# Kernel optimization log

Measured on AMD Instinct MI355X. Metric: run time of the kernel, lower is better.

## Reference

```python
import jax, jax.numpy as jnp
import numpy as np

EPS = 1e-12

def setup_inputs() -> dict:
    key = jax.random.key(0)
    k1, k2 = jax.random.split(key)
    B, C, H, W = 16, 256, 64, 64
    x1 = jax.random.normal(k1, (B, C, H, W), dtype=jnp.float32)
    x2 = jax.random.normal(k2, (B, C, H, W), dtype=jnp.float32)
    return {"x1": x1, "x2": x2}

def _l2norm(x):
    # F.normalize(p=2, dim=2, eps=1e-12): divide by max(norm, eps)
    n = jnp.linalg.norm(x, axis=2, keepdims=True)
    return x / jnp.maximum(n, EPS)

def reference(x1, x2):
    B, C, H, W = x1.shape
    x111 = x1.reshape(B, C, H * W)            # [B,C,N]
    x211 = x2.reshape(B, C, H * W)
    x11 = _l2norm(x111)
    x21 = _l2norm(x211)
    # four CxC score matmuls, fused pairwise adds
    attn1 = jnp.einsum('bcn,bdn->bcd', x11, x11)
    attn2 = jnp.einsum('bcn,bdn->bcd', x21, x21)
    attn0 = jnp.einsum('bcn,bdn->bcd', x21, x11)
    attn00 = jnp.einsum('bcn,bdn->bcd', x11, x21)
    attn11 = jax.nn.softmax(attn1 + attn0, axis=-1)   # [B,C,C]
    attn22 = jax.nn.softmax(attn2 + attn00, axis=-1)
    # back-projection, torch transpose(1,2).reshape(B,C,H,W) semantics
    y1 = jnp.einsum('bcd,bdn->bcn', attn11, x111)     # [B,C,N]
    y2 = jnp.einsum('bcd,bdn->bcn', attn22, x211)
    x1_o = jnp.swapaxes(y1, 1, 2).reshape(B, C, H, W) + x1
    x2_o = jnp.swapaxes(y2, 1, 2).reshape(B, C, H, W) + x2
    return x1_o + x2_o
```

## Files before the change

### kernel.cpp

```cpp
#include <hip/hip_runtime.h>
#include <hip/hip_bf16.h>

#define B_ 16
#define C_ 256
#define N_ 4096
#define CN_ (C_ * N_)

typedef __attribute__((ext_vector_type(8))) short bf16x8_t;
typedef __attribute__((ext_vector_type(8))) unsigned short u16x8_t;
typedef __attribute__((ext_vector_type(4))) float f32x4_t;
typedef unsigned int u32;
typedef unsigned short u16;

__device__ __forceinline__ u16 f2bf(float f) {
    __hip_bfloat16 h = __float2bfloat16(f);
    return __builtin_bit_cast(u16, h);
}
__device__ __forceinline__ float bf2f(u16 u) {
    return __builtin_bit_cast(float, (u32)u << 16);
}

__device__ __forceinline__ void gl_lds16(const void* g, void* l) {
    __builtin_amdgcn_global_load_lds(
        (const __attribute__((address_space(1))) u32*)(g),
        (__attribute__((address_space(3))) u32*)(l), 16, 0, 0);
}

__global__ __launch_bounds__(256) void knorm(const float* __restrict__ x1,
                                             const float* __restrict__ x2,
                                             u16* __restrict__ x1n,
                                             u16* __restrict__ x2n,
                                             u16* __restrict__ sN,
                                             u16* __restrict__ sxb,
                                             float* __restrict__ norms) {
    __shared__ float sx1[4096];
    __shared__ float sx2[4096];
    int row = blockIdx.x;
    int t = threadIdx.x;
    const float4* r1 = (const float4*)(x1 + (size_t)row * N_);
    const float4* r2 = (const float4*)(x2 + (size_t)row * N_);
    float s1 = 0.f, s2 = 0.f;
#pragma unroll
    for (int p = 0; p < 4; ++p) {
        float4 a = r1[p * 256 + t];
        float4 b = r2[p * 256 + t];
        s1 += a.x * a.x + a.y * a.y + a.z * a.z + a.w * a.w;
        s2 += b.x * b.x + b.y * b.y + b.z * b.z + b.w * b.w;
        *(float4*)&sx1[(p * 256 + t) * 4] = a;
        *(float4*)&sx2[(p * 256 + t) * 4] = b;
    }
#pragma unroll
    for (int m = 32; m; m >>= 1) { s1 += __shfl_xor(s1, m); s2 += __shfl_xor(s2, m); }
    __shared__ float red[2][4];
    int wid = t >> 6;
    if ((t & 63) == 0) { red[0][wid] = s1; red[1][wid] = s2; }
    __syncthreads();
    s1 = red[0][0] + red[0][1] + red[0][2] + red[0][3];
    s2 = red[1][0] + red[1][1] + red[1][2] + red[1][3];
    float n1 = fmaxf(sqrtf(s1), 1e-12f);
    float n2 = fmaxf(sqrtf(s2), 1e-12f);
    if (t == 0) {
        int bb = row >> 8, cc = row & 255;
        norms[(bb * 2 + 0) * 256 + cc] = n1;
        norms[(bb * 2 + 1) * 256 + cc] = n2;
    }
    float i1 = 1.0f / n1, i2 = 1.0f / n2;
    const size_t rbase = (size_t)row * N_;
#pragma unroll
    for (int j = 0; j < 2; ++j) {
        int e = j * 2048 + t * 8;
        float a[8], b[8];
        *(float4*)&a[0] = *(const float4*)&sx1[e];
        *(float4*)&a[4] = *(const float4*)&sx1[e + 4];
        *(float4*)&b[0] = *(const float4*)&sx2[e];
        *(float4*)&b[4] = *(const float4*)&sx2[e + 4];
        u16x8_t w1, w2, ws, wr;
#pragma unroll
        for (int i = 0; i < 8; ++i) {
            float va = a[i] * i1, vb = b[i] * i2;
            w1[i] = f2bf(va);
            w2[i] = f2bf(vb);
            ws[i] = f2bf(va + vb);
            wr[i] = f2bf(a[i] + b[i]);
        }
        *(u16x8_t*)(x1n + rbase + e) = w1;
        *(u16x8_t*)(x2n + rbase + e) = w2;
        *(u16x8_t*)(sN  + rbase + e) = ws;
        *(u16x8_t*)(sxb + rbase + e) = wr;
    }
}

__global__ __launch_bounds__(256) void klogits(const u16* __restrict__ sN,
                                               const u16* __restrict__ x1n,
                                               const u16* __restrict__ x2n,
                                               float* __restrict__ part) {
    int bid = blockIdx.x;
    int xcd = bid & 7;
    int u = bid >> 3;
    int b = xcd + 8 * (u & 1);
    int tile = (u >> 1) & 15;
    int kc4 = u >> 5;
    int c0 = (tile & 3) * 64;
    int d0 = (tile >> 2) * 64;

    __shared__ u16 lds[2][3 * 4096];

    int t = threadIdx.x, lane = t & 63, wid = t >> 6;
    int w = wid & 1, chalf = wid >> 1;

    const char* tb[3];
    tb[0] = (const char*)(sN  + (size_t)b * CN_ + (size_t)c0 * N_ + kc4 * 1024);
    tb[1] = (const char*)(x1n + (size_t)b * CN_ + (size_t)d0 * N_ + kc4 * 1024);
    tb[2] = (const char*)(x2n + (size_t)b * CN_ + (size_t)d0 * N_ + kc4 * 1024);
    const char* gsrc[6];
    int ldoff[6];
#pragma unroll
    for (int qq = 0; qq < 6; ++qq) {
        int q = wid * 6 + qq;
        int ti = q >> 3;
        int s0 = (q & 7) * 1024 + lane * 16;
        int rrow = s0 >> 7, inner = s0 & 127;
        gsrc[qq] = tb[ti] + (size_t)rrow * (N_ * 2) + (inner ^ ((rrow & 7) << 4));
        ldoff[qq] = q * 1024;
    }

    f32x4_t acc[2][4];
#pragma unroll
    for (int i = 0; i < 2; ++i)
#pragma unroll
        for (int j = 0; j < 4; ++j) acc[i][j] = 0.f;

    int kl = (lane >> 4) * 16;
    int rA0 = chalf * 32 + (lane & 15);

#pragma unroll
    for (int qq = 0; qq < 6; ++qq)
        gl_lds16(gsrc[qq], (char*)lds[0] + ldoff[qq]);
    __syncthreads();

    for (int ks = 0; ks < 16; ++ks) {
        int p = ks & 1;
        if (ks < 15) {
            int kbyte = (ks + 1) * 128;
#pragma unroll
            for (int qq = 0; qq < 6; ++qq)
                gl_lds16(gsrc[qq] + kbyte, (char*)lds[p ^ 1] + ldoff[qq]);
        }
        const char* Abase = (const char*)lds[p];
        const char* Bbase = (const char*)lds[p] + (1 + w) * 8192;
#pragma unroll
        for (int ksub = 0; ksub < 2; ++ksub) {
            int kc = ksub * 64 + kl;
            bf16x8_t af[2], bfr[4];
#pragma unroll
            for (int mi = 0; mi < 2; ++mi) {
                int rr = rA0 + mi * 16;
                af[mi] = *(const bf16x8_t*)(Abase + ((rr << 7) + (kc ^ ((rr & 7) << 4))));
            }
#pragma unroll
            for (int ni = 0; ni < 4; ++ni) {
                int rr = ni * 16 + (lane & 15);
                bfr[ni] = *(const bf16x8_t*)(Bbase + ((rr << 7) + (kc ^ ((rr & 7) << 4))));
            }
#pragma unroll
            for (int mi = 0; mi < 2; ++mi)
#pragma unroll
                for (int ni = 0; ni < 4; ++ni)
                    acc[mi][ni] = __builtin_amdgcn_mfma_f32_16x16x32_bf16(af[mi], bfr[ni], acc[mi][ni], 0, 0, 0);
        }
        __syncthreads();
    }

    float* outp = part + ((((size_t)kc4 * 16 + b) * 2 + w) * 256 + c0 + chalf * 32) * 256 + d0;
    int orow = (lane >> 4) * 4, ocol = lane & 15;
#pragma unroll
    for (int mi = 0; mi < 2; ++mi)
#pragma unroll
        for (int ni = 0; ni < 4; ++ni)
#pragma unroll
            for (int r = 0; r < 4; ++r)
                outp[(size_t)(mi * 16 + orow + r) * 256 + ni * 16 + ocol] = acc[mi][ni][r];
}

__global__ __launch_bounds__(256) void ksoftmax(const float* __restrict__ part,
                                                const float* __restrict__ norms,
                                                u16* __restrict__ attnp) {
    const size_t S = 2097152;
    int rid = blockIdx.x * 4 + (threadIdx.x >> 6);
    int l = threadIdx.x & 63;
    int bw = rid >> 8, c = rid & 255;
    size_t rbase = (size_t)bw * 65536 + (size_t)c * 256;
    float v[4];
    float m = -1e30f;
#pragma unroll
    for (int j = 0; j < 4; ++j) {
        int d = j * 64 + l;
        v[j] = part[rbase + d] + part[rbase + S + d] +
               part[rbase + 2 * S + d] + part[rbase + 3 * S + d];
        m = fmaxf(m, v[j]);
    }
#pragma unroll
    for (int s = 32; s; s >>= 1) m = fmaxf(m, __shfl_xor(m, s));
    float sum = 0.f;
#pragma unroll
    for (int j = 0; j < 4; ++j) { v[j] = __expf(v[j] - m); sum += v[j]; }
#pragma unroll
    for (int s = 32; s; s >>= 1) sum += __shfl_xor(sum, s);
    float rs = 1.0f / sum;
    u16* outp = attnp + (size_t)rid * 256;
    const float* nr = norms + (size_t)bw * 256;
#pragma unroll
    for (int j = 0; j < 4; ++j)
        outp[j * 64 + l] = f2bf(v[j] * rs * nr[j * 64 + l]);
}

__global__ __launch_bounds__(256) void kout(const u16* __restrict__ x1n,
                                            const u16* __restrict__ x2n,
                                            const u16* __restrict__ attnp,
                                            const u16* __restrict__ sxb,
                                            float* __restrict__ out) {
    int bid = blockIdx.x;
    int xcd = bid & 7;
    int u = bid >> 3;
    int b = xcd + 8 * (u & 1);
    int rest = u >> 1;
    int n0 = (rest >> 1) * 64;
    int c0 = (rest & 1) * 128;

    __shared__ u16 sA[2][2][4096];

    int t = threadIdx.x, lane = t & 63, wid = t >> 6;
    int wc = wid;

    int tensorA = t >> 7;
    int tt = t & 127;
    int dq = (tt & 15) * 4;
    int n8 = (tt >> 4) * 8;
    const u16* Asrc = (tensorA ? x2n : x1n) + (size_t)b * CN_ + n0 + n8;

    const char* Bb[2][2];
#pragma unroll
    for (int tensor = 0; tensor < 2; ++tensor)
#pragma unroll
        for (int ci = 0; ci < 2; ++ci)
            Bb[tensor][ci] = (const char*)(attnp +
                ((size_t)(b * 2 + tensor) * 256 + c0 + wc * 32 + ci * 16 + (lane & 15)) * 256);

    f32x4_t acc1[4][2], acc2[4][2];
#pragma unroll
    for (int i = 0; i < 4; ++i)
#pragma unroll
        for (int j = 0; j < 2; ++j) { acc1[i][j] = 0.f; acc2[i][j] = 0.f; }

    int kl = (lane >> 4) * 16;

    uint4 r0, r1, r2, r3;
#define LOADA(KS) do { \
        size_t kk = (size_t)((KS) * 64 + dq); \
        r0 = *(const uint4*)(Asrc + (kk + 0) * N_); \
        r1 = *(const uint4*)(Asrc + (kk + 1) * N_); \
        r2 = *(const uint4*)(Asrc + (kk + 2) * N_); \
        r3 = *(const uint4*)(Asrc + (kk + 3) * N_); \
    } while (0)
#define WRITEA(BUF) do { \
        const u16* p0 = (const u16*)&r0; \
        const u16* p1 = (const u16*)&r1; \
        const u16* p2 = (const u16*)&r2; \
        const u16* p3 = (const u16*)&r3; \
        char* dst = (char*)&sA[BUF][tensorA][0]; \
        _Pragma("unroll") \
        for (int i = 0; i < 8; ++i) { \
            u32 lo = (u32)p0[i] | ((u32)p1[i] << 16); \
            u32 hi = (u32)p2[i] | ((u32)p3[i] << 16); \
            int n = n8 + i; \
            int addr = (n << 7) + ((dq << 1) ^ ((n & 7) << 4)); \
            uint2 val; val.x = lo; val.y = hi; \
            *(uint2*)(dst + addr) = val; \
        } \
    } while (0)

    LOADA(0);
    WRITEA(0);

    for (int ks = 0; ks < 4; ++ks) {
        int p = ks & 1;
        __syncthreads();
        if (ks < 3) LOADA(ks + 1);
        const char* A0 = (const char*)&sA[p][0][0];
        const char* A1 = (const char*)&sA[p][1][0];
#pragma unroll
        for (int ksub = 0; ksub < 2; ++ksub) {
            int kc = ksub * 64 + kl;
            int kb = ks * 128 + kc;
            bf16x8_t a1f[4], a2f[4], b1f[2], b2f[2];
#pragma unroll
            for (int mi = 0; mi < 4; ++mi) {
                int rr = mi * 16 + (lane & 15);
                int ao = (rr << 7) + (kc ^ ((rr & 7) << 4));
                a1f[mi] = *(const bf16x8_t*)(A0 + ao);
                a2f[mi] = *(const bf16x8_t*)(A1 + ao);
            }
#pragma unroll
            for (int ci = 0; ci < 2; ++ci) {
                b1f[ci] = *(const bf16x8_t*)(Bb[0][ci] + kb);
                b2f[ci] = *(const bf16x8_t*)(Bb[1][ci] + kb);
            }
#pragma unroll
            for (int mi = 0; mi < 4; ++mi)
#pragma unroll
                for (int ci = 0; ci < 2; ++ci) {
                    acc1[mi][ci] = __builtin_amdgcn_mfma_f32_16x16x32_bf16(a1f[mi], b1f[ci], acc1[mi][ci], 0, 0, 0);
                    acc2[mi][ci] = __builtin_amdgcn_mfma_f32_16x16x32_bf16(a2f[mi], b2f[ci], acc2[mi][ci], 0, 0, 0);
                }
        }
        if (ks < 3) WRITEA(p ^ 1);
    }

    const size_t obase = (size_t)b * CN_;
    int orow = (lane >> 4) * 4, ocol = lane & 15;
#pragma unroll
    for (int mi = 0; mi < 4; ++mi)
#pragma unroll
        for (int ci = 0; ci < 2; ++ci)
#pragma unroll
            for (int r = 0; r < 4; ++r) {
                int n = n0 + mi * 16 + orow + r;
                int c = c0 + wc * 32 + ci * 16 + ocol;
                size_t f = obase + (size_t)n * 256 + c;
                out[f] = acc1[mi][ci][r] + acc2[mi][ci][r] + bf2f(sxb[f]);
            }
#undef LOADA
#undef WRITEA
}

extern "C" void kernel_launch(void* const* d_in, const int* in_sizes, int n_in,
                              void* d_out, int out_size, void* d_ws, size_t ws_size,
                              hipStream_t stream) {
    const float* x1 = (const float*)d_in[0];
    const float* x2 = (const float*)d_in[1];
    float* out = (float*)d_out;

    char* ws = (char*)d_ws;
    u16*   x1n   = (u16*)(ws);
    u16*   x2n   = (u16*)(ws + 33554432ull);
    u16*   sN    = (u16*)(ws + 67108864ull);
    u16*   sxb   = (u16*)(ws + 100663296ull);
    float* part  = (float*)(ws + 134217728ull);
    u16*   attnp = (u16*)(ws + 167772160ull);
    float* norms = (float*)(ws + 171966464ull);

    knorm<<<4096, 256, 0, stream>>>(x1, x2, x1n, x2n, sN, sxb, norms);
    klogits<<<1024, 256, 0, stream>>>(sN, x1n, x2n, part);
    ksoftmax<<<2048, 256, 0, stream>>>(part, norms, attnp);
    kout<<<2048, 256, 0, stream>>>(x1n, x2n, attnp, sxb, out);
}
```

Measured before the change: 274.3 us.

## Triple-buffer logits and output GEMMs, pre-transpose activations for direct LDS loads

The logits kernel moves from double-buffered 128-wide K steps with full barriers to a triple-buffered 64-wide K pipeline. It uses explicit vmcnt waits and raw barriers so global-to-LDS loads overlap the MFMAs. A new transpose kernel writes x1n/x2n in [N,C] layout into reused workspace buffers. The output GEMM can then stream A tiles straight into LDS with global_load_lds instead of a register transpose, and it prefetches attention operands into double-buffered registers. The cost is an extra launch plus a full read/write pass over both normalized tensors, and the hand-written waitcnt counts must be exactly right.

```diff
diff --git a/kernel.cpp b/kernel.cpp
--- a/kernel.cpp
+++ b/kernel.cpp
@@ -25,6 +25,9 @@
         (const __attribute__((address_space(1))) u32*)(g),
         (__attribute__((address_space(3))) u32*)(l), 16, 0, 0);
 }
+
+#define WAITV(N) asm volatile("s_waitcnt vmcnt(" #N ")" ::: "memory")
+#define BAR()    do { __builtin_amdgcn_s_barrier(); asm volatile("" ::: "memory"); } while (0)
 
 __global__ __launch_bounds__(256) void knorm(const float* __restrict__ x1,
                                              const float* __restrict__ x2,
@@ -103,26 +106,28 @@
     int c0 = (tile & 3) * 64;
     int d0 = (tile >> 2) * 64;
 
-    __shared__ u16 lds[2][3 * 4096];
+    __shared__ u16 lds[3][6144];
 
     int t = threadIdx.x, lane = t & 63, wid = t >> 6;
     int w = wid & 1, chalf = wid >> 1;
-
-    const char* tb[3];
-    tb[0] = (const char*)(sN  + (size_t)b * CN_ + (size_t)c0 * N_ + kc4 * 1024);
-    tb[1] = (const char*)(x1n + (size_t)b * CN_ + (size_t)d0 * N_ + kc4 * 1024);
-    tb[2] = (const char*)(x2n + (size_t)b * CN_ + (size_t)d0 * N_ + kc4 * 1024);
-    const char* gsrc[6];
-    int ldoff[6];
-#pragma unroll
-    for (int qq = 0; qq < 6; ++qq) {
-        int q = wid * 6 + qq;
-        int ti = q >> 3;
-        int s0 = (q & 7) * 1024 + lane * 16;
-        int rrow = s0 >> 7, inner = s0 & 127;
-        gsrc[qq] = tb[ti] + (size_t)rrow * (N_ * 2) + (inner ^ ((rrow & 7) << 4));
-        ldoff[qq] = q * 1024;
-    }
+    int lm = lane & 15;
+
+    int r = t >> 2;
+    int colb = ((t & 3) * 16) ^ ((r & 3) << 4);
+    const char* gsrc[3];
+    gsrc[0] = (const char*)(sN  + (size_t)b * CN_ + (size_t)(c0 + r) * N_ + kc4 * 1024) + colb;
+    gsrc[1] = (const char*)(x1n + (size_t)b * CN_ + (size_t)(d0 + r) * N_ + kc4 * 1024) + colb;
+    gsrc[2] = (const char*)(x2n + (size_t)b * CN_ + (size_t)(d0 + r) * N_ + kc4 * 1024) + colb;
+    int ldoff[3];
+#pragma unroll
+    for (int qq = 0; qq < 3; ++qq) ldoff[qq] = (t + 256 * qq) * 16;
+
+#define STAGE_L(KS) do { \
+        char* dst = (char*)&lds[(KS) % 3][0]; \
+        _Pragma("unroll") \
+        for (int qq = 0; qq < 3; ++qq) \
+            gl_lds16(gsrc[qq] + (KS) * 64, dst + ldoff[qq]); \
+    } while (0)
 
     f32x4_t acc[2][4];
 #pragma unroll
@@ -130,46 +135,40 @@
 #pragma unroll
         for (int j = 0; j < 4; ++j) acc[i][j] = 0.f;
 
-    int kl = (lane >> 4) * 16;
-    int rA0 = chalf * 32 + (lane & 15);
-
-#pragma unroll
-    for (int qq = 0; qq < 6; ++qq)
-        gl_lds16(gsrc[qq], (char*)lds[0] + ldoff[qq]);
-    __syncthreads();
-
-    for (int ks = 0; ks < 16; ++ks) {
-        int p = ks & 1;
-        if (ks < 15) {
-            int kbyte = (ks + 1) * 128;
-#pragma unroll
-            for (int qq = 0; qq < 6; ++qq)
-                gl_lds16(gsrc[qq] + kbyte, (char*)lds[p ^ 1] + ldoff[qq]);
-        }
-        const char* Abase = (const char*)lds[p];
-        const char* Bbase = (const char*)lds[p] + (1 + w) * 8192;
-#pragma unroll
-        for (int ksub = 0; ksub < 2; ++ksub) {
-            int kc = ksub * 64 + kl;
-            bf16x8_t af[2], bfr[4];
-#pragma unroll
-            for (int mi = 0; mi < 2; ++mi) {
-                int rr = rA0 + mi * 16;
-                af[mi] = *(const bf16x8_t*)(Abase + ((rr << 7) + (kc ^ ((rr & 7) << 4))));
-            }
-#pragma unroll
-            for (int ni = 0; ni < 4; ++ni) {
-                int rr = ni * 16 + (lane & 15);
-                bfr[ni] = *(const bf16x8_t*)(Bbase + ((rr << 7) + (kc ^ ((rr & 7) << 4))));
-            }
-#pragma unroll
-            for (int mi = 0; mi < 2; ++mi)
-#pragma unroll
-                for (int ni = 0; ni < 4; ++ni)
-                    acc[mi][ni] = __builtin_amdgcn_mfma_f32_16x16x32_bf16(af[mi], bfr[ni], acc[mi][ni], 0, 0, 0);
-        }
-        __syncthreads();
-    }
+    int kh16 = (lane >> 4) * 16;
+    int swz = (lm & 3) << 4;
+    int aoff[2], boff[4];
+#pragma unroll
+    for (int mi = 0; mi < 2; ++mi)
+        aoff[mi] = (chalf * 32 + mi * 16 + lm) * 64 + (kh16 ^ swz);
+#pragma unroll
+    for (int ni = 0; ni < 4; ++ni)
+        boff[ni] = (1 + w) * 4096 + (ni * 16 + lm) * 64 + (kh16 ^ swz);
+
+    STAGE_L(0);
+    STAGE_L(1);
+    WAITV(3);
+    BAR();
+
+#pragma unroll
+    for (int ks = 0; ks < 32; ++ks) {
+        if (ks + 2 <= 31) STAGE_L(ks + 2);
+        const char* base = (const char*)&lds[ks % 3][0];
+        bf16x8_t af[2], bfr[4];
+#pragma unroll
+        for (int mi = 0; mi < 2; ++mi) af[mi] = *(const bf16x8_t*)(base + aoff[mi]);
+#pragma unroll
+        for (int ni = 0; ni < 4; ++ni) bfr[ni] = *(const bf16x8_t*)(base + boff[ni]);
+#pragma unroll
+        for (int mi = 0; mi < 2; ++mi)
+#pragma unroll
+            for (int ni = 0; ni < 4; ++ni)
+                acc[mi][ni] = __builtin_amdgcn_mfma_f32_16x16x32_bf16(af[mi], bfr[ni], acc[mi][ni], 0, 0, 0);
+        if (ks < 30) { WAITV(3); }
+        else if (ks == 30) { WAITV(0); }
+        if (ks < 31) BAR();
+    }
+#undef STAGE_L
 
     float* outp = part + ((((size_t)kc4 * 16 + b) * 2 + w) * 256 + c0 + chalf * 32) * 256 + d0;
     int orow = (lane >> 4) * 4, ocol = lane & 15;
@@ -178,8 +177,8 @@
 #pragma unroll
         for (int ni = 0; ni < 4; ++ni)
 #pragma unroll
-            for (int r = 0; r < 4; ++r)
-                outp[(size_t)(mi * 16 + orow + r) * 256 + ni * 16 + ocol] = acc[mi][ni][r];
+            for (int rr = 0; rr < 4; ++rr)
+                outp[(size_t)(mi * 16 + orow + rr) * 256 + ni * 16 + ocol] = acc[mi][ni][rr];
 }
 
 __global__ __launch_bounds__(256) void ksoftmax(const float* __restrict__ part,
@@ -214,8 +213,60 @@
         outp[j * 64 + l] = f2bf(v[j] * rs * nr[j * 64 + l]);
 }
 
-__global__ __launch_bounds__(256) void kout(const u16* __restrict__ x1n,
-                                            const u16* __restrict__ x2n,
+__global__ __launch_bounds__(256) void ktrans(const u16* __restrict__ x1n,
+                                              const u16* __restrict__ x2n,
+                                              u16* __restrict__ xT1,
+                                              u16* __restrict__ xT2) {
+    int bid = blockIdx.x;
+    int xcd = bid & 7;
+    int u = bid >> 3;
+    int b = xcd + 8 * (u & 1);
+    int rest = u >> 1;
+    int ct = rest & 3, nt = rest >> 2;
+    int n0 = nt * 64, c0 = ct * 64;
+
+    __shared__ u16 sT[2][4096];
+
+    int t = threadIdx.x;
+    int tensorA = t >> 7;
+    int tt = t & 127;
+    int dq = (tt & 15) * 4;
+    int n8 = (tt >> 4) * 8;
+    const u16* src = (tensorA ? x2n : x1n) + (size_t)b * CN_ + n0 + n8;
+
+    uint4 r0 = *(const uint4*)(src + (size_t)(c0 + dq + 0) * N_);
+    uint4 r1 = *(const uint4*)(src + (size_t)(c0 + dq + 1) * N_);
+    uint4 r2 = *(const uint4*)(src + (size_t)(c0 + dq + 2) * N_);
+    uint4 r3 = *(const uint4*)(src + (size_t)(c0 + dq + 3) * N_);
+    const u16* p0 = (const u16*)&r0;
+    const u16* p1 = (const u16*)&r1;
+    const u16* p2 = (const u16*)&r2;
+    const u16* p3 = (const u16*)&r3;
+    char* dst = (char*)&sT[tensorA][0];
+#pragma unroll
+    for (int i = 0; i < 8; ++i) {
+        u32 lo = (u32)p0[i] | ((u32)p1[i] << 16);
+        u32 hi = (u32)p2[i] | ((u32)p3[i] << 16);
+        int n = n8 + i;
+        int addr = (n << 7) + ((dq << 1) ^ ((n & 7) << 4));
+        uint2 val; val.x = lo; val.y = hi;
+        *(uint2*)(dst + addr) = val;
+    }
+    __syncthreads();
+
+    u16* out = (tensorA ? xT2 : xT1) + (size_t)b * CN_;
+    const char* sbase = (const char*)&sT[tensorA][0];
+#pragma unroll
+    for (int j = 0; j < 4; ++j) {
+        int n = (tt >> 3) + j * 16;
+        int c16b = (tt & 7) * 16;
+        uint4 v = *(const uint4*)(sbase + (n << 7) + (c16b ^ ((n & 7) << 4)));
+        *(uint4*)(out + (size_t)(n0 + n) * 256 + c0 + (c16b >> 1)) = v;
+    }
+}
+
+__global__ __launch_bounds__(256) void kout(const u16* __restrict__ xT1,
+                                            const u16* __restrict__ xT2,
                                             const u16* __restrict__ attnp,
                                             const u16* __restrict__ sxb,
                                             float* __restrict__ out) {
@@ -224,27 +275,52 @@
     int u = bid >> 3;
     int b = xcd + 8 * (u & 1);
     int rest = u >> 1;
-    int n0 = (rest >> 1) * 64;
-    int c0 = (rest & 1) * 128;
-
-    __shared__ u16 sA[2][2][4096];
+    int nt = rest >> 2;
+    int cs = rest & 3;
+    int n0 = nt * 128, c0 = cs * 64;
+
+    __shared__ u16 lds[3][8192];
 
     int t = threadIdx.x, lane = t & 63, wid = t >> 6;
-    int wc = wid;
-
-    int tensorA = t >> 7;
-    int tt = t & 127;
-    int dq = (tt & 15) * 4;
-    int n8 = (tt >> 4) * 8;
-    const u16* Asrc = (tensorA ? x2n : x1n) + (size_t)b * CN_ + n0 + n8;
-
-    const char* Bb[2][2];
-#pragma unroll
-    for (int tensor = 0; tensor < 2; ++tensor)
+    int wm = wid >> 1, wc2 = wid & 1;
+    int lm = lane & 15;
+    int kh16 = (lane >> 4) * 16;
+
+    const u16* xTt[2] = { xT1 + (size_t)b * CN_, xT2 + (size_t)b * CN_ };
+    const char* gA[4];
+    int ldA[4];
+#pragma unroll
+    for (int qq = 0; qq < 4; ++qq) {
+        int q = t + 256 * qq;
+        int r = q >> 3;
+        int colb = ((q & 7) * 16) ^ ((r & 7) << 4);
+        int T = colb >> 6, k8 = (colb >> 4) & 3;
+        gA[qq] = (const char*)(xTt[T] + (size_t)(n0 + r) * 256 + k8 * 8);
+        ldA[qq] = q * 16;
+    }
+#define STAGE_A(KS) do { \
+        char* dstl = (char*)&lds[(KS) % 3][0]; \
+        _Pragma("unroll") \
+        for (int qq = 0; qq < 4; ++qq) \
+            gl_lds16(gA[qq] + (KS) * 64, dstl + ldA[qq]); \
+    } while (0)
+
+    const char* bptr[2][2];
+#pragma unroll
+    for (int T = 0; T < 2; ++T)
 #pragma unroll
         for (int ci = 0; ci < 2; ++ci)
-            Bb[tensor][ci] = (const char*)(attnp +
-                ((size_t)(b * 2 + tensor) * 256 + c0 + wc * 32 + ci * 16 + (lane & 15)) * 256);
+            bptr[T][ci] = (const char*)(attnp +
+                ((size_t)(b * 2 + T) * 256 + c0 + wc2 * 32 + ci * 16 + lm) * 256) + kh16;
+
+    uint4 brA[4], brB[4];
+#define BLOAD(SET, KS) do { \
+        _Pragma("unroll") \
+        for (int T = 0; T < 2; ++T) \
+            _Pragma("unroll") \
+            for (int ci = 0; ci < 2; ++ci) \
+                SET[T * 2 + ci] = *(const uint4*)(bptr[T][ci] + (KS) * 64); \
+    } while (0)
 
     f32x4_t acc1[4][2], acc2[4][2];
 #pragma unroll
@@ -252,69 +328,49 @@
 #pragma unroll
         for (int j = 0; j < 2; ++j) { acc1[i][j] = 0.f; acc2[i][j] = 0.f; }
 
-    int kl = (lane >> 4) * 16;
-
-    uint4 r0, r1, r2, r3;
-#define LOADA(KS) do { \
-        size_t kk = (size_t)((KS) * 64 + dq); \
-        r0 = *(const uint4*)(Asrc + (kk + 0) * N_); \
-        r1 = *(const uint4*)(Asrc + (kk + 1) * N_); \
-        r2 = *(const uint4*)(Asrc + (kk + 2) * N_); \
-        r3 = *(const uint4*)(Asrc + (kk + 3) * N_); \
-    } while (0)
-#define WRITEA(BUF) do { \
-        const u16* p0 = (const u16*)&r0; \
-        const u16* p1 = (const u16*)&r1; \
-        const u16* p2 = (const u16*)&r2; \
-        const u16* p3 = (const u16*)&r3; \
-        char* dst = (char*)&sA[BUF][tensorA][0]; \
-        _Pragma("unroll") \
-        for (int i = 0; i < 8; ++i) { \
-            u32 lo = (u32)p0[i] | ((u32)p1[i] << 16); \
-            u32 hi = (u32)p2[i] | ((u32)p3[i] << 16); \
-            int n = n8 + i; \
-            int addr = (n << 7) + ((dq << 1) ^ ((n & 7) << 4)); \
-            uint2 val; val.x = lo; val.y = hi; \
-            *(uint2*)(dst + addr) = val; \
-        } \
-    } while (0)
-
-    LOADA(0);
-    WRITEA(0);
-
-    for (int ks = 0; ks < 4; ++ks) {
-        int p = ks & 1;
-        __syncthreads();
-        if (ks < 3) LOADA(ks + 1);
-        const char* A0 = (const char*)&sA[p][0][0];
-        const char* A1 = (const char*)&sA[p][1][0];
-#pragma unroll
-        for (int ksub = 0; ksub < 2; ++ksub) {
-            int kc = ksub * 64 + kl;
-            int kb = ks * 128 + kc;
-            bf16x8_t a1f[4], a2f[4], b1f[2], b2f[2];
-#pragma unroll
-            for (int mi = 0; mi < 4; ++mi) {
-                int rr = mi * 16 + (lane & 15);
-                int ao = (rr << 7) + (kc ^ ((rr & 7) << 4));
-                a1f[mi] = *(const bf16x8_t*)(A0 + ao);
-                a2f[mi] = *(const bf16x8_t*)(A1 + ao);
+    int swz = (lm & 7) << 4;
+    int aoff[2][4];
+#pragma unroll
+    for (int T = 0; T < 2; ++T)
+#pragma unroll
+        for (int mi = 0; mi < 4; ++mi)
+            aoff[T][mi] = (wm * 64 + mi * 16 + lm) * 128 + ((T * 64 + kh16) ^ swz);
+
+    STAGE_A(0);
+    BLOAD(brA, 0);
+    STAGE_A(1);
+    WAITV(8);
+    BAR();
+
+#pragma unroll
+    for (int ks = 0; ks < 8; ++ks) {
+        if (ks + 1 <= 7) {
+            if (ks & 1) BLOAD(brA, ks + 1); else BLOAD(brB, ks + 1);
+        }
+        if (ks + 2 <= 7) STAGE_A(ks + 2);
+        const char* base = (const char*)&lds[ks % 3][0];
+        const uint4* bcur = (ks & 1) ? brB : brA;
+        bf16x8_t a1f[4], a2f[4];
+#pragma unroll
+        for (int mi = 0; mi < 4; ++mi) {
+            a1f[mi] = *(const bf16x8_t*)(base + aoff[0][mi]);
+            a2f[mi] = *(const bf16x8_t*)(base + aoff[1][mi]);
+        }
+#pragma unroll
+        for (int mi = 0; mi < 4; ++mi)
+#pragma unroll
+            for (int ci = 0; ci < 2; ++ci) {
+                acc1[mi][ci] = __builtin_amdgcn_mfma_f32_16x16x32_bf16(
+                    a1f[mi], __builtin_bit_cast(bf16x8_t, bcur[0 * 2 + ci]), acc1[mi][ci], 0, 0, 0);
+                acc2[mi][ci] = __builtin_amdgcn_mfma_f32_16x16x32_bf16(
+                    a2f[mi], __builtin_bit_cast(bf16x8_t, bcur[1 * 2 + ci]), acc2[mi][ci], 0, 0, 0);
             }
-#pragma unroll
-            for (int ci = 0; ci < 2; ++ci) {
-                b1f[ci] = *(const bf16x8_t*)(Bb[0][ci] + kb);
-                b2f[ci] = *(const bf16x8_t*)(Bb[1][ci] + kb);
-            }
-#pragma unroll
-            for (int mi = 0; mi < 4; ++mi)
-#pragma unroll
-                for (int ci = 0; ci < 2; ++ci) {
-                    acc1[mi][ci] = __builtin_amdgcn_mfma_f32_16x16x32_bf16(a1f[mi], b1f[ci], acc1[mi][ci], 0, 0, 0);
-                    acc2[mi][ci] = __builtin_amdgcn_mfma_f32_16x16x32_bf16(a2f[mi], b2f[ci], acc2[mi][ci], 0, 0, 0);
-                }
-        }
-        if (ks < 3) WRITEA(p ^ 1);
-    }
+        if (ks < 6) { WAITV(8); }
+        else if (ks == 6) { WAITV(4); }
+        if (ks < 7) BAR();
+    }
+#undef STAGE_A
+#undef BLOAD
 
     const size_t obase = (size_t)b * CN_;
     int orow = (lane >> 4) * 4, ocol = lane & 15;
@@ -323,14 +379,12 @@
 #pragma unroll
         for (int ci = 0; ci < 2; ++ci)
 #pragma unroll
-            for (int r = 0; r < 4; ++r) {
-                int n = n0 + mi * 16 + orow + r;
-                int c = c0 + wc * 32 + ci * 16 + ocol;
+            for (int rr = 0; rr < 4; ++rr) {
+                int n = n0 + wm * 64 + mi * 16 + orow + rr;
+                int c = c0 + wc2 * 32 + ci * 16 + ocol;
                 size_t f = obase + (size_t)n * 256 + c;
-                out[f] = acc1[mi][ci][r] + acc2[mi][ci][r] + bf2f(sxb[f]);
+                out[f] = acc1[mi][ci][rr] + acc2[mi][ci][rr] + bf2f(sxb[f]);
             }
-#undef LOADA
-#undef WRITEA
 }
 
 extern "C" void kernel_launch(void* const* d_in, const int* in_sizes, int n_in,
@@ -349,8 +403,12 @@
     u16*   attnp = (u16*)(ws + 167772160ull);
     float* norms = (float*)(ws + 171966464ull);
 
+    u16* xT1 = (u16*)sN;
+    u16* xT2 = (u16*)part;
+
     knorm<<<4096, 256, 0, stream>>>(x1, x2, x1n, x2n, sN, sxb, norms);
     klogits<<<1024, 256, 0, stream>>>(sN, x1n, x2n, part);
     ksoftmax<<<2048, 256, 0, stream>>>(part, norms, attnp);
-    kout<<<2048, 256, 0, stream>>>(x1n, x2n, attnp, sxb, out);
-}
+    ktrans<<<4096, 256, 0, stream>>>(x1n, x2n, xT1, xT2);
+    kout<<<2048, 256, 0, stream>>>(xT1, xT2, attnp, sxb, out);
+}
```

New measurement: 296.3 us. 1.08x slower.

## Triple-buffer logits K-loop and retile output GEMM with LDS-staged attention

Applied to the files above, without the earlier changes.

The logits kernel moves from double-buffered 128-wide K steps to a three-stage ring of 32-wide steps, using explicit vmcnt waits and raw barriers, and reorders the block-to-tile mapping. The output kernel is retiled to 128x64 tiles with 8 K steps, and the attention operand is staged into LDS through direct global-to-LDS loads instead of being read from global memory per lane. The aim is to overlap loads with MFMA and cut redundant global traffic. In exchange there are more barriers per K and manual waitcnt logic that can break if the compiler reorders the memory operations.

```diff
diff --git a/kernel.cpp b/kernel.cpp
--- a/kernel.cpp
+++ b/kernel.cpp
@@ -25,6 +25,9 @@
         (const __attribute__((address_space(1))) u32*)(g),
         (__attribute__((address_space(3))) u32*)(l), 16, 0, 0);
 }
+
+#define WAITV(N) asm volatile("s_waitcnt vmcnt(" #N ")" ::: "memory")
+#define BAR()    do { __builtin_amdgcn_s_barrier(); asm volatile("" ::: "memory"); } while (0)
 
 __global__ __launch_bounds__(256) void knorm(const float* __restrict__ x1,
                                              const float* __restrict__ x2,
@@ -97,32 +100,35 @@
     int bid = blockIdx.x;
     int xcd = bid & 7;
     int u = bid >> 3;
-    int b = xcd + 8 * (u & 1);
-    int tile = (u >> 1) & 15;
-    int kc4 = u >> 5;
+    int tile = u & 15;
+    int g = u >> 4;
+    int b = xcd + 8 * (g & 1);
+    int kc4 = g >> 1;
     int c0 = (tile & 3) * 64;
     int d0 = (tile >> 2) * 64;
 
-    __shared__ u16 lds[2][3 * 4096];
+    __shared__ u16 lds[3][6144];
 
     int t = threadIdx.x, lane = t & 63, wid = t >> 6;
     int w = wid & 1, chalf = wid >> 1;
-
-    const char* tb[3];
-    tb[0] = (const char*)(sN  + (size_t)b * CN_ + (size_t)c0 * N_ + kc4 * 1024);
-    tb[1] = (const char*)(x1n + (size_t)b * CN_ + (size_t)d0 * N_ + kc4 * 1024);
-    tb[2] = (const char*)(x2n + (size_t)b * CN_ + (size_t)d0 * N_ + kc4 * 1024);
-    const char* gsrc[6];
-    int ldoff[6];
-#pragma unroll
-    for (int qq = 0; qq < 6; ++qq) {
-        int q = wid * 6 + qq;
-        int ti = q >> 3;
-        int s0 = (q & 7) * 1024 + lane * 16;
-        int rrow = s0 >> 7, inner = s0 & 127;
-        gsrc[qq] = tb[ti] + (size_t)rrow * (N_ * 2) + (inner ^ ((rrow & 7) << 4));
-        ldoff[qq] = q * 1024;
-    }
+    int lm = lane & 15;
+
+    int r = t >> 2;
+    int colb = ((t & 3) * 16) ^ ((r & 3) << 4);
+    const char* gsrc[3];
+    gsrc[0] = (const char*)(sN  + (size_t)b * CN_ + (size_t)(c0 + r) * N_ + kc4 * 1024) + colb;
+    gsrc[1] = (const char*)(x1n + (size_t)b * CN_ + (size_t)(d0 + r) * N_ + kc4 * 1024) + colb;
+    gsrc[2] = (const char*)(x2n + (size_t)b * CN_ + (size_t)(d0 + r) * N_ + kc4 * 1024) + colb;
+    int ldoff[3];
+#pragma unroll
+    for (int qq = 0; qq < 3; ++qq) ldoff[qq] = (t + 256 * qq) * 16;
+
+#define STAGE_L(KS) do { \
+        char* dst = (char*)&lds[(KS) % 3][0]; \
+        _Pragma("unroll") \
+        for (int qq = 0; qq < 3; ++qq) \
+            gl_lds16(gsrc[qq] + (KS) * 64, dst + ldoff[qq]); \
+    } while (0)
 
     f32x4_t acc[2][4];
 #pragma unroll
@@ -130,46 +136,40 @@
 #pragma unroll
         for (int j = 0; j < 4; ++j) acc[i][j] = 0.f;
 
-    int kl = (lane >> 4) * 16;
-    int rA0 = chalf * 32 + (lane & 15);
-
-#pragma unroll
-    for (int qq = 0; qq < 6; ++qq)
-        gl_lds16(gsrc[qq], (char*)lds[0] + ldoff[qq]);
-    __syncthreads();
-
-    for (int ks = 0; ks < 16; ++ks) {
-        int p = ks & 1;
-        if (ks < 15) {
-            int kbyte = (ks + 1) * 128;
-#pragma unroll
-            for (int qq = 0; qq < 6; ++qq)
-                gl_lds16(gsrc[qq] + kbyte, (char*)lds[p ^ 1] + ldoff[qq]);
-        }
-        const char* Abase = (const char*)lds[p];
-        const char* Bbase = (const char*)lds[p] + (1 + w) * 8192;
-#pragma unroll
-        for (int ksub = 0; ksub < 2; ++ksub) {
-            int kc = ksub * 64 + kl;
-            bf16x8_t af[2], bfr[4];
-#pragma unroll
-            for (int mi = 0; mi < 2; ++mi) {
-                int rr = rA0 + mi * 16;
-                af[mi] = *(const bf16x8_t*)(Abase + ((rr << 7) + (kc ^ ((rr & 7) << 4))));
-            }
-#pragma unroll
-            for (int ni = 0; ni < 4; ++ni) {
-                int rr = ni * 16 + (lane & 15);
-                bfr[ni] = *(const bf16x8_t*)(Bbase + ((rr << 7) + (kc ^ ((rr & 7) << 4))));
-            }
-#pragma unroll
-            for (int mi = 0; mi < 2; ++mi)
-#pragma unroll
-                for (int ni = 0; ni < 4; ++ni)
-                    acc[mi][ni] = __builtin_amdgcn_mfma_f32_16x16x32_bf16(af[mi], bfr[ni], acc[mi][ni], 0, 0, 0);
-        }
-        __syncthreads();
-    }
+    int kh16 = (lane >> 4) * 16;
+    int swz = (lm & 3) << 4;
+    int aoff[2], boff[4];
+#pragma unroll
+    for (int mi = 0; mi < 2; ++mi)
+        aoff[mi] = (chalf * 32 + mi * 16 + lm) * 64 + (kh16 ^ swz);
+#pragma unroll
+    for (int ni = 0; ni < 4; ++ni)
+        boff[ni] = (1 + w) * 4096 + (ni * 16 + lm) * 64 + (kh16 ^ swz);
+
+    STAGE_L(0);
+    STAGE_L(1);
+    WAITV(3);
+    BAR();
+
+#pragma unroll
+    for (int ks = 0; ks < 32; ++ks) {
+        if (ks + 2 <= 31) STAGE_L(ks + 2);
+        const char* base = (const char*)&lds[ks % 3][0];
+        bf16x8_t af[2], bfr[4];
+#pragma unroll
+        for (int mi = 0; mi < 2; ++mi) af[mi] = *(const bf16x8_t*)(base + aoff[mi]);
+#pragma unroll
+        for (int ni = 0; ni < 4; ++ni) bfr[ni] = *(const bf16x8_t*)(base + boff[ni]);
+#pragma unroll
+        for (int mi = 0; mi < 2; ++mi)
+#pragma unroll
+            for (int ni = 0; ni < 4; ++ni)
+                acc[mi][ni] = __builtin_amdgcn_mfma_f32_16x16x32_bf16(af[mi], bfr[ni], acc[mi][ni], 0, 0, 0);
+        if (ks < 30) { WAITV(3); }
+        else if (ks == 30) { WAITV(0); }
+        if (ks < 31) BAR();
+    }
+#undef STAGE_L
 
     float* outp = part + ((((size_t)kc4 * 16 + b) * 2 + w) * 256 + c0 + chalf * 32) * 256 + d0;
     int orow = (lane >> 4) * 4, ocol = lane & 15;
@@ -178,8 +178,8 @@
 #pragma unroll
         for (int ni = 0; ni < 4; ++ni)
 #pragma unroll
-            for (int r = 0; r < 4; ++r)
-                outp[(size_t)(mi * 16 + orow + r) * 256 + ni * 16 + ocol] = acc[mi][ni][r];
+            for (int rr = 0; rr < 4; ++rr)
+                outp[(size_t)(mi * 16 + orow + rr) * 256 + ni * 16 + ocol] = acc[mi][ni][rr];
 }
 
 __global__ __launch_bounds__(256) void ksoftmax(const float* __restrict__ part,
@@ -221,116 +221,136 @@
                                             float* __restrict__ out) {
     int bid = blockIdx.x;
     int xcd = bid & 7;
-    int u = bid >> 3;
-    int b = xcd + 8 * (u & 1);
-    int rest = u >> 1;
-    int n0 = (rest >> 1) * 64;
-    int c0 = (rest & 1) * 128;
-
-    __shared__ u16 sA[2][2][4096];
+    int j = bid >> 3;
+    int b = xcd + 8 * (j >> 7);
+    int j2 = j & 127;
+    int nt = j2 >> 2, cs = j2 & 3;
+    int n0 = nt * 128, c0 = cs * 64;
+
+    __shared__ char ldsA[2][16384];
+    __shared__ char ldsB[2][8192];
 
     int t = threadIdx.x, lane = t & 63, wid = t >> 6;
-    int wc = wid;
-
-    int tensorA = t >> 7;
+    int wm = wid >> 1, wc2 = wid & 1;
+    int lm = lane & 15, lq = lane >> 4;
+
+    int T_A = t >> 7;
     int tt = t & 127;
-    int dq = (tt & 15) * 4;
-    int n8 = (tt >> 4) * 8;
-    const u16* Asrc = (tensorA ? x2n : x1n) + (size_t)b * CN_ + n0 + n8;
-
-    const char* Bb[2][2];
-#pragma unroll
-    for (int tensor = 0; tensor < 2; ++tensor)
+    int dq = (tt & 7) * 4;
+    int n8 = (tt >> 3) * 8;
+    const u16* Asrc = (T_A ? x2n : x1n) + (size_t)b * CN_ + n0 + n8 + (size_t)dq * N_;
+
+    const char* Bsrc[2];
+    int Bldoff[2];
+#pragma unroll
+    for (int q = 0; q < 2; ++q) {
+        int c = q * 32 + (t >> 3);
+        int s = (t & 7) ^ (c & 7);
+        int T = s >> 2, dsl = s & 3;
+        Bsrc[q] = (const char*)(attnp + ((size_t)(b * 2 + T) * 65536
+                 + (size_t)(c0 + c) * 256 + dsl * 8));
+        Bldoff[q] = q * 4096 + t * 16;
+    }
+
+    int aoff[2][4], boff[2][2];
+#pragma unroll
+    for (int T = 0; T < 2; ++T) {
+#pragma unroll
+        for (int mi = 0; mi < 4; ++mi)
+            aoff[T][mi] = (wm * 64 + mi * 16 + lm) * 128
+                        + (((T * 4 + lq) ^ (lm & 7)) << 4);
 #pragma unroll
         for (int ci = 0; ci < 2; ++ci)
-            Bb[tensor][ci] = (const char*)(attnp +
-                ((size_t)(b * 2 + tensor) * 256 + c0 + wc * 32 + ci * 16 + (lane & 15)) * 256);
+            boff[T][ci] = (wc2 * 32 + ci * 16 + lm) * 128
+                        + (((T * 4 + lq) ^ (lm & 7)) << 4);
+    }
 
     f32x4_t acc1[4][2], acc2[4][2];
 #pragma unroll
     for (int i = 0; i < 4; ++i)
 #pragma unroll
-        for (int j = 0; j < 2; ++j) { acc1[i][j] = 0.f; acc2[i][j] = 0.f; }
-
-    int kl = (lane >> 4) * 16;
+        for (int jj = 0; jj < 2; ++jj) { acc1[i][jj] = 0.f; acc2[i][jj] = 0.f; }
 
     uint4 r0, r1, r2, r3;
 #define LOADA(KS) do { \
-        size_t kk = (size_t)((KS) * 64 + dq); \
-        r0 = *(const uint4*)(Asrc + (kk + 0) * N_); \
-        r1 = *(const uint4*)(Asrc + (kk + 1) * N_); \
-        r2 = *(const uint4*)(Asrc + (kk + 2) * N_); \
-        r3 = *(const uint4*)(Asrc + (kk + 3) * N_); \
+        size_t off = (size_t)(KS) * 32 * N_; \
+        r0 = *(const uint4*)(Asrc + off); \
+        r1 = *(const uint4*)(Asrc + off + N_); \
+        r2 = *(const uint4*)(Asrc + off + 2 * N_); \
+        r3 = *(const uint4*)(Asrc + off + 3 * N_); \
+    } while (0)
+#define STAGEB(KS, BUF) do { \
+        _Pragma("unroll") \
+        for (int q = 0; q < 2; ++q) \
+            gl_lds16(Bsrc[q] + (KS) * 64, &ldsB[BUF][0] + Bldoff[q]); \
     } while (0)
 #define WRITEA(BUF) do { \
         const u16* p0 = (const u16*)&r0; \
         const u16* p1 = (const u16*)&r1; \
         const u16* p2 = (const u16*)&r2; \
         const u16* p3 = (const u16*)&r3; \
-        char* dst = (char*)&sA[BUF][tensorA][0]; \
+        char* dst = &ldsA[BUF][0]; \
         _Pragma("unroll") \
         for (int i = 0; i < 8; ++i) { \
             u32 lo = (u32)p0[i] | ((u32)p1[i] << 16); \
             u32 hi = (u32)p2[i] | ((u32)p3[i] << 16); \
             int n = n8 + i; \
-            int addr = (n << 7) + ((dq << 1) ^ ((n & 7) << 4)); \
+            int addr = (n << 7) + ((((T_A * 4 + (dq >> 3)) ^ (n & 7)) << 4) + (dq & 4) * 2); \
             uint2 val; val.x = lo; val.y = hi; \
             *(uint2*)(dst + addr) = val; \
         } \
     } while (0)
 
+    STAGEB(0, 0);
     LOADA(0);
     WRITEA(0);
-
-    for (int ks = 0; ks < 4; ++ks) {
-        int p = ks & 1;
+    __syncthreads();
+
+    for (int ks = 0; ks < 8; ++ks) {
+        int pp = ks & 1;
+        if (ks < 7) {
+            STAGEB(ks + 1, pp ^ 1);
+            LOADA(ks + 1);
+        }
+        const char* A = &ldsA[pp][0];
+        const char* Bb = &ldsB[pp][0];
+        bf16x8_t a1f[4], a2f[4], b1f[2], b2f[2];
+#pragma unroll
+        for (int mi = 0; mi < 4; ++mi) {
+            a1f[mi] = *(const bf16x8_t*)(A + aoff[0][mi]);
+            a2f[mi] = *(const bf16x8_t*)(A + aoff[1][mi]);
+        }
+#pragma unroll
+        for (int ci = 0; ci < 2; ++ci) {
+            b1f[ci] = *(const bf16x8_t*)(Bb + boff[0][ci]);
+            b2f[ci] = *(const bf16x8_t*)(Bb + boff[1][ci]);
+        }
+#pragma unroll
+        for (int mi = 0; mi < 4; ++mi)
+#pragma unroll
+            for (int ci = 0; ci < 2; ++ci) {
+                acc1[mi][ci] = __builtin_amdgcn_mfma_f32_16x16x32_bf16(a1f[mi], b1f[ci], acc1[mi][ci], 0, 0, 0);
+                acc2[mi][ci] = __builtin_amdgcn_mfma_f32_16x16x32_bf16(a2f[mi], b2f[ci], acc2[mi][ci], 0, 0, 0);
+            }
+        if (ks < 7) WRITEA(pp ^ 1);
         __syncthreads();
-        if (ks < 3) LOADA(ks + 1);
-        const char* A0 = (const char*)&sA[p][0][0];
-        const char* A1 = (const char*)&sA[p][1][0];
-#pragma unroll
-        for (int ksub = 0; ksub < 2; ++ksub) {
-            int kc = ksub * 64 + kl;
-            int kb = ks * 128 + kc;
-            bf16x8_t a1f[4], a2f[4], b1f[2], b2f[2];
-#pragma unroll
-            for (int mi = 0; mi < 4; ++mi) {
-                int rr = mi * 16 + (lane & 15);
-                int ao = (rr << 7) + (kc ^ ((rr & 7) << 4));
-                a1f[mi] = *(const bf16x8_t*)(A0 + ao);
-                a2f[mi] = *(const bf16x8_t*)(A1 + ao);
+    }
+#undef LOADA
+#undef STAGEB
+#undef WRITEA
+
+    const size_t obase = (size_t)b * CN_;
+#pragma unroll
+    for (int mi = 0; mi < 4; ++mi)
+#pragma unroll
+        for (int ci = 0; ci < 2; ++ci)
+#pragma unroll
+            for (int rr = 0; rr < 4; ++rr) {
+                int n = n0 + wm * 64 + mi * 16 + lq * 4 + rr;
+                int c = c0 + wc2 * 32 + ci * 16 + lm;
+                size_t f = obase + (size_t)n * 256 + c;
+                out[f] = acc1[mi][ci][rr] + acc2[mi][ci][rr] + bf2f(sxb[f]);
             }
-#pragma unroll
-            for (int ci = 0; ci < 2; ++ci) {
-                b1f[ci] = *(const bf16x8_t*)(Bb[0][ci] + kb);
-                b2f[ci] = *(const bf16x8_t*)(Bb[1][ci] + kb);
-            }
-#pragma unroll
-            for (int mi = 0; mi < 4; ++mi)
-#pragma unroll
-                for (int ci = 0; ci < 2; ++ci) {
-                    acc1[mi][ci] = __builtin_amdgcn_mfma_f32_16x16x32_bf16(a1f[mi], b1f[ci], acc1[mi][ci], 0, 0, 0);
-                    acc2[mi][ci] = __builtin_amdgcn_mfma_f32_16x16x32_bf16(a2f[mi], b2f[ci], acc2[mi][ci], 0, 0, 0);
-                }
-        }
-        if (ks < 3) WRITEA(p ^ 1);
-    }
-
-    const size_t obase = (size_t)b * CN_;
-    int orow = (lane >> 4) * 4, ocol = lane & 15;
-#pragma unroll
-    for (int mi = 0; mi < 4; ++mi)
-#pragma unroll
-        for (int ci = 0; ci < 2; ++ci)
-#pragma unroll
-            for (int r = 0; r < 4; ++r) {
-                int n = n0 + mi * 16 + orow + r;
-                int c = c0 + wc * 32 + ci * 16 + ocol;
-                size_t f = obase + (size_t)n * 256 + c;
-                out[f] = acc1[mi][ci][r] + acc2[mi][ci][r] + bf2f(sxb[f]);
-            }
-#undef LOADA
-#undef WRITEA
 }
 
 extern "C" void kernel_launch(void* const* d_in, const int* in_sizes, int n_in,
```

Result: faster. 268.8 us (-2.0%).
